# Performance work log

Hardware: AMD Instinct MI355X
Metric: run time of the kernel (lower is better)

The kernel has to match this reference:

```python
import jax, jax.numpy as jnp
import numpy as np

N, M, B, C, L, H = 8192, 8192, 16, 512, 64, 8
HEAD_DIM = C // H
PER_BATCH_KEYS = M // B
MASK_VAL = -1000.0  # matches torch masked_fill_ value


def setup_inputs() -> dict:
    key0 = jax.random.key(0)
    ks = jax.random.split(key0, 8)
    query = jax.random.normal(ks[0], (N, C), jnp.float32)
    key = jax.random.normal(ks[1], (M, C), jnp.float32)
    value = jax.random.normal(ks[2], (M, C), jnp.float32)
    # xavier-ish init for projections
    in_proj_weight = jax.random.normal(ks[3], (3 * C, C), jnp.float32) * (1.0 / np.sqrt(C))
    in_proj_bias = jnp.zeros((3 * C,), jnp.float32)
    out_w = jax.random.normal(ks[4], (C, C), jnp.float32) * (1.0 / np.sqrt(C))
    out_b = jnp.zeros((C,), jnp.float32)
    index_pair = jax.random.randint(ks[5], (N, L), 0, PER_BATCH_KEYS).astype(jnp.int32)
    pad = jax.random.uniform(ks[6], (N, L)) < 0.05
    index_pair = jnp.where(pad, jnp.int32(-1), index_pair)
    query_batch_cnt = jnp.full((B,), N // B, jnp.int32)
    key_batch_cnt = jnp.full((B,), PER_BATCH_KEYS, jnp.int32)
    index_pair_batch = jnp.repeat(jnp.arange(B, dtype=jnp.int32), N // B)
    return {
        "query": query, "key": key, "value": value,
        "in_proj_weight": in_proj_weight, "in_proj_bias": in_proj_bias,
        "out_w": out_w, "out_b": out_b,
        "index_pair": index_pair, "query_batch_cnt": query_batch_cnt,
        "key_batch_cnt": key_batch_cnt, "index_pair_batch": index_pair_batch,
    }


def reference(query, key, value, in_proj_weight, in_proj_bias, out_w, out_b,
              index_pair, query_batch_cnt, key_batch_cnt, index_pair_batch):
    embed_dim = query.shape[-1]
    scaling = float(HEAD_DIM) ** -0.5
    # qkv projections (in_proj_weight is [3C, C], applied as F.linear => x @ W.T + b)
    q = (query @ in_proj_weight[:embed_dim].T + in_proj_bias[:embed_dim]) * scaling
    k = key @ in_proj_weight[embed_dim:2 * embed_dim].T + in_proj_bias[embed_dim:2 * embed_dim]
    v = value @ in_proj_weight[2 * embed_dim:].T + in_proj_bias[2 * embed_dim:]
    q = q.reshape(N, H, HEAD_DIM)
    k = k.reshape(M, H, HEAD_DIM)
    v = v.reshape(M, H, HEAD_DIM)
    # local -> global key indices: offset by start of each query's batch key block
    key_start = jnp.cumsum(key_batch_cnt) - key_batch_cnt          # (B,)
    offset = key_start[index_pair_batch]                            # (N,)
    valid = index_pair >= 0                                         # (N, L)
    gidx = jnp.where(valid, index_pair + offset[:, None], 0)        # (N, L), safe gather
    # gather-based scores: (N, L, H)
    scores = jnp.einsum("nhd,nlhd->nlh", q, k[gidx])
    scores = jnp.where(valid[..., None], scores, MASK_VAL)
    w = jax.nn.softmax(scores, axis=1)                              # softmax over neighbors L
    # weighted value sum; masked weights underflow to exactly 0 in fp32
    attn = jnp.einsum("nlh,nlhd->nhd", w, v[gidx]).reshape(N, embed_dim)
    attn = attn @ out_w.T + out_b
    return attn, w.sum(axis=-1) / H
```

## Files before the change

### kernel.cpp

```cpp
#include <hip/hip_runtime.h>
#include <hip/hip_bf16.h>
#include <math.h>

#define NQ 8192
#define MK 8192
#define CD 512
#define LN 64
#define HH 8
#define HD 64
#define BB 16
#define KPB 512
#define QPB 512

typedef short short8 __attribute__((ext_vector_type(8)));
typedef float floatx4 __attribute__((ext_vector_type(4)));

__device__ __forceinline__ unsigned short f2bf(float x) {
    unsigned int u = __builtin_bit_cast(unsigned int, x);
    return (unsigned short)((u + 0x7FFFu + ((u >> 16) & 1u)) >> 16);
}
__device__ __forceinline__ unsigned int pkbf(float lo, float hi) {
    float2 f; f.x = lo; f.y = hi;
    __hip_bfloat162 h2 = __float22bfloat162_rn(f);
    unsigned int u;
    __builtin_memcpy(&u, &h2, 4);
    return u;
}
__device__ __forceinline__ float bflo(unsigned int u) {
    return __builtin_bit_cast(float, u << 16);
}
__device__ __forceinline__ float bfhij(unsigned int u) {
    return __builtin_bit_cast(float, u);
}
__device__ __forceinline__ short8 u4s8(uint4 u) {
    short8 s; __builtin_memcpy(&s, &u, 16); return s;
}
__device__ __forceinline__ float exp2v(float x) {
    float r; asm("v_exp_f32 %0, %1" : "=v"(r) : "v"(x)); return r;
}
__device__ __forceinline__ float rcpv(float x) {
    float r; asm("v_rcp_f32 %0, %1" : "=v"(r) : "v"(x)); return r;
}

__device__ __forceinline__ void gl_lds16(const unsigned short* g, unsigned short* l) {
    __builtin_amdgcn_global_load_lds(
        (const __attribute__((address_space(1))) unsigned int*)g,
        (__attribute__((address_space(3))) unsigned int*)l, 16, 0, 0);
}

struct ConvSeg { const float* src; unsigned short* dst; int n4; };
struct ConvArgs { ConvSeg s[5]; };

__global__ __launch_bounds__(256) void convert_bf16(ConvArgs a) {
    const int seg = blockIdx.y;
    const int i = blockIdx.x * 256 + threadIdx.x;
    if (i >= a.s[seg].n4) return;
    const float4 v = ((const float4*)a.s[seg].src)[i];
    uint2 o; o.x = pkbf(v.x, v.y); o.y = pkbf(v.z, v.w);
    ((uint2*)a.s[seg].dst)[i] = o;
}

__device__ __forceinline__ void gemm_bf_body(const unsigned short* __restrict__ A,
                                             const unsigned short* __restrict__ W,
                                             const float* __restrict__ bias,
                                             float* __restrict__ outf,
                                             unsigned short* __restrict__ outb,
                                             float scale) {
    __shared__ unsigned short As[64 * 64];
    __shared__ unsigned short Bs[128 * 64];

    const int tid  = threadIdx.x;
    const int row0 = blockIdx.x * 64;
    const int col0 = blockIdx.y * 128;

    const int w    = tid >> 6;
    const int lane = tid & 63;
    const int q    = lane >> 4;
    const int ml   = lane & 15;

    const int sr = lane >> 3;
    const int sg = (lane & 7) ^ sr;
    const unsigned short* Ap = A + (size_t)(row0 + w * 16 + sr) * CD + sg * 8;
    const unsigned short* Wp = W + (size_t)(col0 + w * 32 + sr) * CD + sg * 8;
    unsigned short* Asw = &As[(w * 16) * 64];
    unsigned short* Bsw = &Bs[(w * 32) * 64];

    floatx4 acc[4][2];
#pragma unroll
    for (int i = 0; i < 4; ++i)
#pragma unroll
        for (int j = 0; j < 2; ++j)
            acc[i][j] = (floatx4){0.f, 0.f, 0.f, 0.f};

    for (int k0 = 0; k0 < CD; k0 += 64) {
        __syncthreads();
#pragma unroll
        for (int i = 0; i < 2; ++i)
            gl_lds16(Ap + (size_t)(i * 8) * CD + k0, Asw + i * 8 * 64);
#pragma unroll
        for (int i = 0; i < 4; ++i)
            gl_lds16(Wp + (size_t)(i * 8) * CD + k0, Bsw + i * 8 * 64);
        __syncthreads();

#pragma unroll
        for (int kw = 0; kw < 2; ++kw) {
            short8 af[4], bf[2];
            const int gp = ((kw * 4 + q) ^ (ml & 7)) * 8;
#pragma unroll
            for (int mi = 0; mi < 4; ++mi)
                af[mi] = *(const short8*)&As[(mi * 16 + ml) * 64 + gp];
#pragma unroll
            for (int ni = 0; ni < 2; ++ni)
                bf[ni] = *(const short8*)&Bs[(w * 32 + ni * 16 + ml) * 64 + gp];
#pragma unroll
            for (int mi = 0; mi < 4; ++mi)
#pragma unroll
                for (int ni = 0; ni < 2; ++ni)
                    acc[mi][ni] = __builtin_amdgcn_mfma_f32_16x16x32_bf16(
                        af[mi], bf[ni], acc[mi][ni], 0, 0, 0);
        }
    }

    float bv[2];
#pragma unroll
    for (int ni = 0; ni < 2; ++ni)
        bv[ni] = bias[col0 + w * 32 + ni * 16 + ml];
#pragma unroll
    for (int mi = 0; mi < 4; ++mi) {
#pragma unroll
        for (int ni = 0; ni < 2; ++ni) {
            const int cg = col0 + w * 32 + ni * 16 + ml;
#pragma unroll
            for (int rr = 0; rr < 4; ++rr) {
                const int rg = row0 + mi * 16 + q * 4 + rr;
                const float val = (acc[mi][ni][rr] + bv[ni]) * scale;
                if (outb) outb[(size_t)rg * CD + cg] = f2bf(val);
                else      outf[(size_t)rg * CD + cg] = val;
            }
        }
    }
}

#define QSCALE 0.18033688011112042f

__global__ __launch_bounds__(256) void qkv_gemm(const unsigned short* __restrict__ A_bf,
                                                const unsigned short* __restrict__ w_bf,
                                                const float* __restrict__ bias,
                                                unsigned short* __restrict__ q_bf,
                                                unsigned short* __restrict__ k_bf,
                                                unsigned short* __restrict__ v_bf) {
    const int z = blockIdx.z;
    const unsigned short* A = A_bf + (size_t)z * NQ * CD;
    unsigned short* outb = (z == 0) ? q_bf : ((z == 1) ? k_bf : v_bf);
    gemm_bf_body(A, w_bf + (size_t)z * CD * CD, bias + (size_t)z * CD,
                 nullptr, outb, (z == 0) ? QSCALE : 1.0f);
}

__global__ __launch_bounds__(256) void out_gemm(const unsigned short* __restrict__ A,
                                                const unsigned short* __restrict__ W,
                                                const float* __restrict__ bias,
                                                float* __restrict__ out) {
    gemm_bf_body(A, W, bias, out, nullptr, 1.0f);
}

#define MFMA16(a, b, c) __builtin_amdgcn_mfma_f32_16x16x32_bf16(a, b, c, 0, 0, 0)
#define MK_ -1000.0f


#define FMA8(u, wgt) do {                                                     \
    const float w_ = (wgt);                                                   \
    a0 = fmaf(w_, bflo((u).x),  a0);  a1 = fmaf(w_, bfhij((u).x), a1);        \
    a2 = fmaf(w_, bflo((u).y),  a2);  a3 = fmaf(w_, bfhij((u).y), a3);        \
    a4 = fmaf(w_, bflo((u).z),  a4);  a5 = fmaf(w_, bfhij((u).z), a5);        \
    a6 = fmaf(w_, bflo((u).w),  a6);  a7 = fmaf(w_, bfhij((u).w), a7);        \
} while (0)

#define KRD(row, ch) (*(const uint4*)&K_s[(row) * 64 + ((((ch) ^ ((row) & 7))) * 8)])
#define VRD(row, ch) (*(const uint4*)&V_s[(row) * 64 + ((((ch) ^ ((row) & 7))) * 8)])

__global__ __launch_bounds__(512, 2) void attn_kernel(
    const unsigned short* __restrict__ q_bf,
    const unsigned short* __restrict__ k_bf,
    const unsigned short* __restrict__ v_bf,
    const int* __restrict__ index_pair,
    const int* __restrict__ key_batch_cnt,
    unsigned short* __restrict__ attn_bf,
    float* __restrict__ W8) {
    const int tid  = threadIdx.x;
    const int wid  = tid >> 6;
    const int lane = tid & 63;
    const int bid  = blockIdx.x;
    const int pair = bid & 127;
    const int qt   = bid >> 7;
    const int head = pair & 7;
    const int batch= pair >> 3;

    const int quad = lane >> 4, ml = lane & 15;
    const int r8 = lane >> 3, c8 = lane & 7;

    __shared__ unsigned short K_s[KPB * 64];
    __shared__ unsigned short V_s[KPB * 64];
    __shared__ int   g_s[8 * 64];
    __shared__ float w_st[8 * 64];
    __shared__ float red_s[8 * 64 * 9];

    int cnt = (lane < BB) ? key_batch_cnt[lane] : 0;
#pragma unroll
    for (int d = 1; d < BB; d <<= 1) {
        const int t = __shfl_up(cnt, d, 64);
        if (lane >= d) cnt += t;
    }
    const int off0 = (batch > 0) ? __shfl(cnt, batch - 1, 64) : 0;

#pragma unroll
    for (int j = 0; j < 8; ++j) {
        const int rowb = wid * 64 + j * 8;
        const size_t grow = (size_t)(off0 + rowb + r8);
        gl_lds16(k_bf + grow * CD + head * HD + ((c8 ^ r8) * 8), &K_s[rowb * 64]);
        gl_lds16(v_bf + grow * CD + head * HD + ((c8 ^ r8) * 8), &V_s[rowb * 64]);
    }
    __syncthreads();

    const int n0 = batch * QPB + qt * 128 + wid * 16;
    const bool p0 = ml & 1, p1 = ml & 2, p2 = ml & 4, p3 = ml & 8;
    const int jpub = (ml >> 2) * 16 + quad * 4 + (ml & 3);
    int*   gs  = &g_s[wid * 64];
    float* wst = &w_st[wid * 64];
    float* red = &red_s[wid * 64 * 9];

    int idx = index_pair[(size_t)n0 * LN + lane];
    for (int qi = 0; qi < 16; ++qi) {
        const int n = n0 + qi;
        const int idx_next = (qi < 15) ? index_pair[(size_t)(n + 1) * LN + lane] : 0;

        const unsigned long long vmask = __ballot(idx >= 0);
        const int g = (idx >= 0) ? idx : 0;
        gs[lane] = g;

        const int krow0 = __shfl(g, ml, 64);
        const int krow1 = __shfl(g, 16 + ml, 64);
        const int krow2 = __shfl(g, 32 + ml, 64);
        const int krow3 = __shfl(g, 48 + ml, 64);

        const unsigned long long tb = vmask >> (quad * 4);
        const unsigned mybits =
            (unsigned)( (tb & 0xFull)
                      | (((tb >> 16) & 0xFull) << 4)
                      | (((tb >> 32) & 0xFull) << 8)
                      | (((tb >> 48) & 0xFull) << 12));
        const bool b0  = mybits & 1u,          b1  = (mybits >> 1) & 1u;
        const bool b2  = (mybits >> 2) & 1u,   b3  = (mybits >> 3) & 1u;
        const bool b4  = (mybits >> 4) & 1u,   b5  = (mybits >> 5) & 1u;
        const bool b6  = (mybits >> 6) & 1u,   b7  = (mybits >> 7) & 1u;
        const bool b8  = (mybits >> 8) & 1u,   b9  = (mybits >> 9) & 1u;
        const bool b10 = (mybits >> 10) & 1u,  b11 = (mybits >> 11) & 1u;
        const bool b12 = (mybits >> 12) & 1u,  b13 = (mybits >> 13) & 1u;
        const bool b14 = (mybits >> 14) & 1u,  b15 = (mybits >> 15) & 1u;

        const unsigned short* qrow = q_bf + (size_t)n * CD + head * HD;
        const uint4 qa0 = *(const uint4*)(qrow + quad * 8);
        const uint4 qa1 = *(const uint4*)(qrow + 32 + quad * 8);

        const uint4 kf00 = KRD(krow0, quad), kf01 = KRD(krow0, 4 + quad);
        const uint4 kf10 = KRD(krow1, quad), kf11 = KRD(krow1, 4 + quad);
        const uint4 kf20 = KRD(krow2, quad), kf21 = KRD(krow2, 4 + quad);
        const uint4 kf30 = KRD(krow3, quad), kf31 = KRD(krow3, 4 + quad);

        floatx4 z0 = (floatx4){0.f,0.f,0.f,0.f}, z1 = z0, z2 = z0, z3 = z0;
        z0 = MFMA16(u4s8(kf00), u4s8(qa0), z0);
        z0 = MFMA16(u4s8(kf01), u4s8(qa1), z0);
        z1 = MFMA16(u4s8(kf10), u4s8(qa0), z1);
        z1 = MFMA16(u4s8(kf11), u4s8(qa1), z1);
        z2 = MFMA16(u4s8(kf20), u4s8(qa0), z2);
        z2 = MFMA16(u4s8(kf21), u4s8(qa1), z2);
        z3 = MFMA16(u4s8(kf30), u4s8(qa0), z3);
        z3 = MFMA16(u4s8(kf31), u4s8(qa1), z3);

        float s00 = b0  ? z0[0] : MK_,  s01 = b1  ? z0[1] : MK_;
        float s02 = b2  ? z0[2] : MK_,  s03 = b3  ? z0[3] : MK_;
        float s04 = b4  ? z1[0] : MK_,  s05 = b5  ? z1[1] : MK_;
        float s06 = b6  ? z1[2] : MK_,  s07 = b7  ? z1[3] : MK_;
        float s08 = b8  ? z2[0] : MK_,  s09 = b9  ? z2[1] : MK_;
        float s10 = b10 ? z2[2] : MK_,  s11 = b11 ? z2[3] : MK_;
        float s12 = b12 ? z3[0] : MK_,  s13 = b13 ? z3[1] : MK_;
        float s14 = b14 ? z3[2] : MK_,  s15 = b15 ? z3[3] : MK_;
        float mx = fmaxf(fmaxf(fmaxf(fmaxf(s00, s01), fmaxf(s02, s03)),
                               fmaxf(fmaxf(s04, s05), fmaxf(s06, s07))),
                         fmaxf(fmaxf(fmaxf(s08, s09), fmaxf(s10, s11)),
                               fmaxf(fmaxf(s12, s13), fmaxf(s14, s15))));
        mx = fmaxf(mx, __shfl_xor(mx, 16, 64));
        mx = fmaxf(mx, __shfl_xor(mx, 32, 64));
        s00 = exp2v(s00 - mx); s01 = exp2v(s01 - mx);
        s02 = exp2v(s02 - mx); s03 = exp2v(s03 - mx);
        s04 = exp2v(s04 - mx); s05 = exp2v(s05 - mx);
        s06 = exp2v(s06 - mx); s07 = exp2v(s07 - mx);
        s08 = exp2v(s08 - mx); s09 = exp2v(s09 - mx);
        s10 = exp2v(s10 - mx); s11 = exp2v(s11 - mx);
        s12 = exp2v(s12 - mx); s13 = exp2v(s13 - mx);
        s14 = exp2v(s14 - mx); s15 = exp2v(s15 - mx);
        float sm = (((s00 + s01) + (s02 + s03)) + ((s04 + s05) + (s06 + s07)))
                 + (((s08 + s09) + (s10 + s11)) + ((s12 + s13) + (s14 + s15)));
        sm += __shfl_xor(sm, 16, 64);
        sm += __shfl_xor(sm, 32, 64);
        const float rs = rcpv(sm);
        const float t0 = p1 ? (p0 ? s03 : s02) : (p0 ? s01 : s00);
        const float t1 = p1 ? (p0 ? s07 : s06) : (p0 ? s05 : s04);
        const float t2 = p1 ? (p0 ? s11 : s10) : (p0 ? s09 : s08);
        const float t3 = p1 ? (p0 ? s15 : s14) : (p0 ? s13 : s12);
        const float pick = p3 ? (p2 ? t3 : t2) : (p2 ? t1 : t0);
        const float w = pick * rs;
        wst[jpub] = w;
        W8[((size_t)head * NQ + n) * LN + jpub] = w * 0.125f;

        const int   vr0 = gs[0 * 8 + r8], vr1 = gs[1 * 8 + r8];
        const int   vr2 = gs[2 * 8 + r8], vr3 = gs[3 * 8 + r8];
        const int   vr4 = gs[4 * 8 + r8], vr5 = gs[5 * 8 + r8];
        const int   vr6 = gs[6 * 8 + r8], vr7 = gs[7 * 8 + r8];
        const float wv0 = wst[0 * 8 + r8], wv1 = wst[1 * 8 + r8];
        const float wv2 = wst[2 * 8 + r8], wv3 = wst[3 * 8 + r8];
        const float wv4 = wst[4 * 8 + r8], wv5 = wst[5 * 8 + r8];
        const float wv6 = wst[6 * 8 + r8], wv7 = wst[7 * 8 + r8];
        const uint4 vv0 = VRD(vr0, c8);
        const uint4 vv1 = VRD(vr1, c8);
        const uint4 vv2 = VRD(vr2, c8);
        const uint4 vv3 = VRD(vr3, c8);
        const uint4 vv4 = VRD(vr4, c8);
        const uint4 vv5 = VRD(vr5, c8);
        const uint4 vv6 = VRD(vr6, c8);
        const uint4 vv7 = VRD(vr7, c8);
        float a0 = 0.f, a1 = 0.f, a2 = 0.f, a3 = 0.f;
        float a4 = 0.f, a5 = 0.f, a6 = 0.f, a7 = 0.f;
        FMA8(vv0, wv0); FMA8(vv1, wv1); FMA8(vv2, wv2); FMA8(vv3, wv3);
        FMA8(vv4, wv4); FMA8(vv5, wv5); FMA8(vv6, wv6); FMA8(vv7, wv7);

        red[lane * 9 + 0] = a0; red[lane * 9 + 1] = a1;
        red[lane * 9 + 2] = a2; red[lane * 9 + 3] = a3;
        red[lane * 9 + 4] = a4; red[lane * 9 + 5] = a5;
        red[lane * 9 + 6] = a6; red[lane * 9 + 7] = a7;
        const int bcol = lane >> 3, e = lane & 7;
        const float s = (((red[(0 * 8 + bcol) * 9 + e] + red[(1 * 8 + bcol) * 9 + e])
                        + (red[(2 * 8 + bcol) * 9 + e] + red[(3 * 8 + bcol) * 9 + e]))
                       + ((red[(4 * 8 + bcol) * 9 + e] + red[(5 * 8 + bcol) * 9 + e])
                        + (red[(6 * 8 + bcol) * 9 + e] + red[(7 * 8 + bcol) * 9 + e])));
        attn_bf[(size_t)n * CD + head * HD + lane] = f2bf(s);

        idx = idx_next;
    }
}

__global__ __launch_bounds__(256) void out2_reduce(const float* __restrict__ W8,
                                                   float* __restrict__ out2) {
    const size_t i = (size_t)blockIdx.x * 256 + threadIdx.x;
    float s = 0.f;
#pragma unroll
    for (int h = 0; h < HH; ++h) s += W8[(size_t)h * NQ * LN + i];
    out2[i] = s;
}

extern "C" void kernel_launch(void* const* d_in, const int* in_sizes, int n_in,
                              void* d_out, int out_size, void* d_ws, size_t ws_size,
                              hipStream_t stream) {
    const float* query   = (const float*)d_in[0];
    const float* key     = (const float*)d_in[1];
    const float* value   = (const float*)d_in[2];
    const float* ipw     = (const float*)d_in[3];
    const float* ipb     = (const float*)d_in[4];
    const float* out_w   = (const float*)d_in[5];
    const float* out_b   = (const float*)d_in[6];
    const int*   index_pair       = (const int*)d_in[7];
    const int*   key_batch_cnt    = (const int*)d_in[9];

    float* out = (float*)d_out;
    unsigned short* q_bf  = (unsigned short*)d_ws;
    unsigned short* k_bf  = q_bf + (size_t)NQ * CD;
    unsigned short* v_bf  = k_bf + (size_t)NQ * CD;
    unsigned short* A_bf  = v_bf + (size_t)NQ * CD;
    unsigned short* w_bf  = A_bf + (size_t)3 * NQ * CD;
    unsigned short* ow_bf = w_bf + (size_t)3 * CD * CD;
    unsigned short* attn_bf = A_bf;
    float* W8 = (float*)(A_bf + (size_t)NQ * CD);

    ConvArgs ca;
    ca.s[0] = {query, A_bf,                       NQ * CD / 4};
    ca.s[1] = {key,   A_bf + (size_t)NQ * CD,     NQ * CD / 4};
    ca.s[2] = {value, A_bf + (size_t)2 * NQ * CD, NQ * CD / 4};
    ca.s[3] = {ipw,   w_bf,                       3 * CD * CD / 4};
    ca.s[4] = {out_w, ow_bf,                      CD * CD / 4};
    dim3 g0(NQ * CD / 4 / 256, 5);
    convert_bf16<<<g0, 256, 0, stream>>>(ca);

    dim3 g1(NQ / 64, CD / 128, 3);
    qkv_gemm<<<g1, 256, 0, stream>>>(A_bf, w_bf, ipb, q_bf, k_bf, v_bf);

    attn_kernel<<<512, 512, 0, stream>>>(q_bf, k_bf, v_bf, index_pair,
                                         key_batch_cnt, attn_bf, W8);

    out2_reduce<<<NQ * LN / 256, 256, 0, stream>>>(W8, out + (size_t)NQ * CD);

    dim3 g3(NQ / 64, CD / 128, 1);
    out_gemm<<<g3, 256, 0, stream>>>(attn_bf, ow_bf, out_b, out);
}
```

Before: 212.5 us.

## Enlarge QKV GEMM row tile and fuse weight-sum reduction into out GEMM launch

Measured after the change: 199.1 us. -6.3%, faster.

```diff
diff --git a/kernel.cpp b/kernel.cpp
--- a/kernel.cpp
+++ b/kernel.cpp
@@ -60,17 +60,18 @@
     ((uint2*)a.s[seg].dst)[i] = o;
 }
 
+template<int MI>
 __device__ __forceinline__ void gemm_bf_body(const unsigned short* __restrict__ A,
                                              const unsigned short* __restrict__ W,
                                              const float* __restrict__ bias,
                                              float* __restrict__ outf,
                                              unsigned short* __restrict__ outb,
                                              float scale) {
-    __shared__ unsigned short As[64 * 64];
+    __shared__ unsigned short As[MI * 16 * 64];
     __shared__ unsigned short Bs[128 * 64];
 
     const int tid  = threadIdx.x;
-    const int row0 = blockIdx.x * 64;
+    const int row0 = blockIdx.x * (MI * 16);
     const int col0 = blockIdx.y * 128;
 
     const int w    = tid >> 6;
@@ -80,14 +81,14 @@
 
     const int sr = lane >> 3;
     const int sg = (lane & 7) ^ sr;
-    const unsigned short* Ap = A + (size_t)(row0 + w * 16 + sr) * CD + sg * 8;
+    const unsigned short* Ap = A + (size_t)(row0 + w * (MI * 4) + sr) * CD + sg * 8;
     const unsigned short* Wp = W + (size_t)(col0 + w * 32 + sr) * CD + sg * 8;
-    unsigned short* Asw = &As[(w * 16) * 64];
+    unsigned short* Asw = &As[(w * (MI * 4)) * 64];
     unsigned short* Bsw = &Bs[(w * 32) * 64];
 
-    floatx4 acc[4][2];
-#pragma unroll
-    for (int i = 0; i < 4; ++i)
+    floatx4 acc[MI][2];
+#pragma unroll
+    for (int i = 0; i < MI; ++i)
 #pragma unroll
         for (int j = 0; j < 2; ++j)
             acc[i][j] = (floatx4){0.f, 0.f, 0.f, 0.f};
@@ -95,7 +96,7 @@
     for (int k0 = 0; k0 < CD; k0 += 64) {
         __syncthreads();
 #pragma unroll
-        for (int i = 0; i < 2; ++i)
+        for (int i = 0; i < MI / 2; ++i)
             gl_lds16(Ap + (size_t)(i * 8) * CD + k0, Asw + i * 8 * 64);
 #pragma unroll
         for (int i = 0; i < 4; ++i)
@@ -104,16 +105,16 @@
 
 #pragma unroll
         for (int kw = 0; kw < 2; ++kw) {
-            short8 af[4], bf[2];
+            short8 af[MI], bf[2];
             const int gp = ((kw * 4 + q) ^ (ml & 7)) * 8;
 #pragma unroll
-            for (int mi = 0; mi < 4; ++mi)
+            for (int mi = 0; mi < MI; ++mi)
                 af[mi] = *(const short8*)&As[(mi * 16 + ml) * 64 + gp];
 #pragma unroll
             for (int ni = 0; ni < 2; ++ni)
                 bf[ni] = *(const short8*)&Bs[(w * 32 + ni * 16 + ml) * 64 + gp];
 #pragma unroll
-            for (int mi = 0; mi < 4; ++mi)
+            for (int mi = 0; mi < MI; ++mi)
 #pragma unroll
                 for (int ni = 0; ni < 2; ++ni)
                     acc[mi][ni] = __builtin_amdgcn_mfma_f32_16x16x32_bf16(
@@ -126,7 +127,7 @@
     for (int ni = 0; ni < 2; ++ni)
         bv[ni] = bias[col0 + w * 32 + ni * 16 + ml];
 #pragma unroll
-    for (int mi = 0; mi < 4; ++mi) {
+    for (int mi = 0; mi < MI; ++mi) {
 #pragma unroll
         for (int ni = 0; ni < 2; ++ni) {
             const int cg = col0 + w * 32 + ni * 16 + ml;
@@ -143,24 +144,38 @@
 
 #define QSCALE 0.18033688011112042f
 
-__global__ __launch_bounds__(256) void qkv_gemm(const unsigned short* __restrict__ A_bf,
-                                                const unsigned short* __restrict__ w_bf,
-                                                const float* __restrict__ bias,
-                                                unsigned short* __restrict__ q_bf,
-                                                unsigned short* __restrict__ k_bf,
-                                                unsigned short* __restrict__ v_bf) {
+__global__ __launch_bounds__(256, 3) void qkv_gemm(const unsigned short* __restrict__ A_bf,
+                                                   const unsigned short* __restrict__ w_bf,
+                                                   const float* __restrict__ bias,
+                                                   unsigned short* __restrict__ q_bf,
+                                                   unsigned short* __restrict__ k_bf,
+                                                   unsigned short* __restrict__ v_bf) {
     const int z = blockIdx.z;
     const unsigned short* A = A_bf + (size_t)z * NQ * CD;
     unsigned short* outb = (z == 0) ? q_bf : ((z == 1) ? k_bf : v_bf);
-    gemm_bf_body(A, w_bf + (size_t)z * CD * CD, bias + (size_t)z * CD,
-                 nullptr, outb, (z == 0) ? QSCALE : 1.0f);
+    gemm_bf_body<8>(A, w_bf + (size_t)z * CD * CD, bias + (size_t)z * CD,
+                    nullptr, outb, (z == 0) ? QSCALE : 1.0f);
 }
 
 __global__ __launch_bounds__(256) void out_gemm(const unsigned short* __restrict__ A,
                                                 const unsigned short* __restrict__ W,
                                                 const float* __restrict__ bias,
-                                                float* __restrict__ out) {
-    gemm_bf_body(A, W, bias, out, nullptr, 1.0f);
+                                                float* __restrict__ out,
+                                                const float* __restrict__ W8,
+                                                float* __restrict__ out2) {
+    if (blockIdx.y == 4) {
+        const size_t base = (size_t)blockIdx.x * 4096 + threadIdx.x;
+#pragma unroll
+        for (int t = 0; t < 16; ++t) {
+            const size_t i = base + (size_t)t * 256;
+            float s = 0.f;
+#pragma unroll
+            for (int h = 0; h < HH; ++h) s += W8[(size_t)h * NQ * LN + i];
+            out2[i] = s;
+        }
+        return;
+    }
+    gemm_bf_body<4>(A, W, bias, out, nullptr, 1.0f);
 }
 
 #define MFMA16(a, b, c) __builtin_amdgcn_mfma_f32_16x16x32_bf16(a, b, c, 0, 0, 0)
@@ -348,15 +363,6 @@
     }
 }
 
-__global__ __launch_bounds__(256) void out2_reduce(const float* __restrict__ W8,
-                                                   float* __restrict__ out2) {
-    const size_t i = (size_t)blockIdx.x * 256 + threadIdx.x;
-    float s = 0.f;
-#pragma unroll
-    for (int h = 0; h < HH; ++h) s += W8[(size_t)h * NQ * LN + i];
-    out2[i] = s;
-}
-
 extern "C" void kernel_launch(void* const* d_in, const int* in_sizes, int n_in,
                               void* d_out, int out_size, void* d_ws, size_t ws_size,
                               hipStream_t stream) {
@@ -389,14 +395,13 @@
     dim3 g0(NQ * CD / 4 / 256, 5);
     convert_bf16<<<g0, 256, 0, stream>>>(ca);
 
-    dim3 g1(NQ / 64, CD / 128, 3);
+    dim3 g1(NQ / 128, CD / 128, 3);
     qkv_gemm<<<g1, 256, 0, stream>>>(A_bf, w_bf, ipb, q_bf, k_bf, v_bf);
 
     attn_kernel<<<512, 512, 0, stream>>>(q_bf, k_bf, v_bf, index_pair,
                                          key_batch_cnt, attn_bf, W8);
 
-    out2_reduce<<<NQ * LN / 256, 256, 0, stream>>>(W8, out + (size_t)NQ * CD);
-
-    dim3 g3(NQ / 64, CD / 128, 1);
-    out_gemm<<<g3, 256, 0, stream>>>(attn_bf, ow_bf, out_b, out);
-}
+    dim3 g3(NQ / 64, 5, 1);
+    out_gemm<<<g3, 256, 0, stream>>>(attn_bf, ow_bf, out_b, out,
+                                     W8, out + (size_t)NQ * CD);
+}
```
